# Performance work log

Measured on AMD Instinct MI355X. Metric: run time of the kernel, lower is better.

## Reference

```python
import jax, jax.numpy as jnp
import numpy as np

NUM_GRAPHS = 128

def _gcn_conv(x, W, b, src, dst, deg_inv_sqrt, n_nodes):
    # PyG GCNConv: h = X W; out[dst] += d^-1/2[src] * d^-1/2[dst] * h[src]; out += b
    h = x @ W
    norm = deg_inv_sqrt[src] * deg_inv_sqrt[dst]  # [E]
    msg = h[src] * norm[:, None]                  # [E, C]
    out = jax.ops.segment_sum(msg, dst, num_segments=n_nodes)
    return out + b


def setup_inputs() -> dict:
    key = jax.random.key(0)
    k1, k2, k3, k4, k5 = jax.random.split(key, 5)
    n_nodes, n_edges, c_in, c_hid = 50000, 800000, 256, 256
    x = jax.random.normal(k1, (n_nodes, c_in), dtype=jnp.float32)
    edge_index = jax.random.randint(k2, (2, n_edges), 0, n_nodes, dtype=jnp.int64)
    batch = jnp.sort(jax.random.randint(k3, (n_nodes,), 0, NUM_GRAPHS, dtype=jnp.int64))
    s1 = 1.0 / np.sqrt(c_in)
    s2 = 1.0 / np.sqrt(c_hid)
    W1 = jax.random.uniform(k4, (c_in, c_hid), jnp.float32, -s1, s1)
    b1 = jnp.zeros((c_hid,), jnp.float32)
    W2 = jax.random.uniform(k5, (c_hid, c_hid), jnp.float32, -s2, s2)
    b2 = jnp.zeros((c_hid,), jnp.float32)
    return {"x": x, "edge_index": edge_index, "batch": batch,
            "W1": W1, "b1": b1, "W2": W2, "b2": b2}


def reference(x, edge_index, batch, W1, b1, W2, b2):
    n_nodes = x.shape[0]
    # add self-loops (GCNConv default add_self_loops=True)
    loops = jnp.arange(n_nodes, dtype=edge_index.dtype)
    src = jnp.concatenate([edge_index[0], loops])
    dst = jnp.concatenate([edge_index[1], loops])
    deg = jax.ops.segment_sum(jnp.ones_like(dst, dtype=x.dtype), dst, num_segments=n_nodes)
    deg_inv_sqrt = jnp.where(deg > 0, jax.lax.rsqrt(deg), 0.0)

    h = jax.nn.relu(_gcn_conv(x, W1, b1, src, dst, deg_inv_sqrt, n_nodes))
    # dropout p=0.2 is identity in eval mode
    h = jax.nn.relu(_gcn_conv(h, W2, b2, src, dst, deg_inv_sqrt, n_nodes))

    # global mean pool over graph ids
    sums = jax.ops.segment_sum(h, batch, num_segments=NUM_GRAPHS)
    cnts = jax.ops.segment_sum(jnp.ones((n_nodes,), h.dtype), batch, num_segments=NUM_GRAPHS)
    return sums / jnp.maximum(cnts, 1.0)[:, None]
```

## Files before the change

### kernel.cpp

```cpp
#include <hip/hip_runtime.h>

#define NCH 256
#define NS  16

typedef short short8 __attribute__((ext_vector_type(8)));
typedef float f32x4  __attribute__((ext_vector_type(4)));

__device__ __forceinline__ float b2f(unsigned short u) {
    union { unsigned int i; float f; } x; x.i = ((unsigned int)u) << 16; return x.f;
}
__device__ __forceinline__ unsigned short f2b(float f) {
    unsigned int u = __float_as_uint(f);
    unsigned int r = (u + 0x7FFFu + ((u >> 16) & 1u)) >> 16;
    return (unsigned short)r;
}

__global__ __launch_bounds__(256) void k_init_deg(int* __restrict__ deg, int n) {
    int i = blockIdx.x * 256 + threadIdx.x;
    if (i < n) deg[i] = 1;
}

__global__ __launch_bounds__(256) void k_hist(const int* __restrict__ dst, int E,
                                              int* __restrict__ deg) {
    int e = blockIdx.x * 256 + threadIdx.x;
    if (e < E) atomicAdd(&deg[dst[e]], 1);
}

__global__ __launch_bounds__(256) void k_scan_blk(const int* __restrict__ deg,
                                                  int* __restrict__ part,
                                                  int* __restrict__ bsum, int N) {
    __shared__ int sm[256];
    int t = threadIdx.x;
    int base = blockIdx.x * 1024 + t * 4;
    int v[4]; int s = 0;
#pragma unroll
    for (int j = 0; j < 4; ++j) {
        int i = base + j;
        int d = (i < N) ? (deg[i] - 1) : 0;
        v[j] = d; s += d;
    }
    sm[t] = s; __syncthreads();
#pragma unroll
    for (int off = 1; off < 256; off <<= 1) {
        int u = (t >= off) ? sm[t - off] : 0;
        __syncthreads();
        sm[t] += u;
        __syncthreads();
    }
    int excl = sm[t] - s;
#pragma unroll
    for (int j = 0; j < 4; ++j) {
        int i = base + j;
        if (i < N) part[i] = excl;
        excl += v[j];
    }
    if (t == 255) bsum[blockIdx.x] = sm[255];
}

__global__ void k_scan_top(int* __restrict__ bsum, int nb, int* __restrict__ rowptr_end) {
    int t = threadIdx.x;
    int orig = (t < nb) ? bsum[t] : 0;
    int v = orig;
#pragma unroll
    for (int off = 1; off < 64; off <<= 1) {
        int u = __shfl_up(v, off, 64);
        if (t >= off) v += u;
    }
    if (t < nb) bsum[t] = v - orig;
    if (t == 63) *rowptr_end = v;
}

__global__ __launch_bounds__(256) void k_finalize(const int* __restrict__ deg,
                                                  int* __restrict__ row_ptr,
                                                  const int* __restrict__ boff,
                                                  int* __restrict__ cursor,
                                                  float* __restrict__ dinv, int N) {
    int i = blockIdx.x * 256 + threadIdx.x;
    if (i < N) {
        int rp = row_ptr[i] + boff[i >> 10];
        row_ptr[i] = rp;
        cursor[i]  = rp;
        dinv[i] = rsqrtf((float)deg[i]);
    }
}

__global__ __launch_bounds__(256) void k_scatter(const int* __restrict__ src,
                                                 const int* __restrict__ dst, int E,
                                                 int* __restrict__ cursor,
                                                 int* __restrict__ col) {
    int e = blockIdx.x * 256 + threadIdx.x;
    if (e < E) {
        int d = dst[e];
        int pos = atomicAdd(&cursor[d], 1);
        col[pos] = src[e];
    }
}

__global__ __launch_bounds__(256) void k_wprep(const int* __restrict__ col,
                                               const float* __restrict__ dinv,
                                               int2* __restrict__ cw, int E) {
    int i = blockIdx.x * 256 + threadIdx.x;
    if (i < E) {
        int s = col[i];
        cw[i] = make_int2(s, __float_as_int(dinv[s]));
    }
}

__global__ __launch_bounds__(256) void k_cast8(const float* __restrict__ in,
                                               unsigned short* __restrict__ out, int n8) {
    int i = blockIdx.x * 256 + threadIdx.x;
    if (i < n8) {
        const float4* p = (const float4*)(in + (size_t)i * 8);
        float4 a = p[0], b = p[1];
        unsigned short us[8];
        us[0] = f2b(a.x); us[1] = f2b(a.y); us[2] = f2b(a.z); us[3] = f2b(a.w);
        us[4] = f2b(b.x); us[5] = f2b(b.y); us[6] = f2b(b.z); us[7] = f2b(b.w);
        *(int4*)(out + (size_t)i * 8) = *(const int4*)us;
    }
}

__global__ __launch_bounds__(256) void k_castT(const float* __restrict__ W1,
                                               const float* __restrict__ W2,
                                               unsigned short* __restrict__ Wt1,
                                               unsigned short* __restrict__ Wt2) {
    int k = blockIdx.x, n = threadIdx.x;
    const float* W = blockIdx.y ? W2 : W1;
    unsigned short* Wt = blockIdx.y ? Wt2 : Wt1;
    Wt[(size_t)n * 256 + k] = f2b(W[(size_t)k * 256 + n]);
}

__device__ __forceinline__ void a_load(const unsigned short* __restrict__ A,
                                       int tile, int M, int lr, int ku, short8* dst) {
    int row = tile * 16 + lr; if (row >= M) row = M - 1;
    const unsigned short* pa = A + (size_t)row * NCH + ku * 8;
#pragma unroll
    for (int ks = 0; ks < 8; ++ks) dst[ks] = *(const short8*)(pa + ks * 32);
}

__global__ __launch_bounds__(256, 2) void k_gemm_rs(const unsigned short* __restrict__ A,
                                                    const unsigned short* __restrict__ Bt,
                                                    unsigned short* __restrict__ C, int M) {
    const int tid  = threadIdx.x;
    const int wid  = tid >> 6;
    const int lane = tid & 63;
    const int lr   = lane & 15;
    const int ku   = lane >> 4;

    short8 bfr[4][8];
    {
        const unsigned short* pb = Bt + (size_t)(wid * 64 + lr) * NCH + ku * 8;
#pragma unroll
        for (int nf = 0; nf < 4; ++nf)
#pragma unroll
            for (int ks = 0; ks < 8; ++ks)
                bfr[nf][ks] = *(const short8*)(pb + nf * 16 * NCH + ks * 32);
    }

    const int tiles = (M + 15) >> 4;
    int t = blockIdx.x;

    short8 afA[8], afB[8];
    if (t < tiles) a_load(A, t, M, lr, ku, afA);

    for (; t < tiles; t += gridDim.x) {
        int tn = t + gridDim.x;
        if (tn < tiles) a_load(A, tn, M, lr, ku, afB);

        f32x4 acc[4];
#pragma unroll
        for (int nf = 0; nf < 4; ++nf) acc[nf] = (f32x4){0.f, 0.f, 0.f, 0.f};

#pragma unroll
        for (int ks = 0; ks < 8; ++ks)
#pragma unroll
            for (int nf = 0; nf < 4; ++nf)
                acc[nf] = __builtin_amdgcn_mfma_f32_16x16x32_bf16(afA[ks], bfr[nf][ks],
                                                                  acc[nf], 0, 0, 0);

        int rb = t * 16 + ku * 4;
#pragma unroll
        for (int nf = 0; nf < 4; ++nf) {
            int col = wid * 64 + nf * 16 + lr;
#pragma unroll
            for (int r = 0; r < 4; ++r) {
                int row = rb + r;
                if (row < M) C[(size_t)row * NCH + col] = f2b(acc[nf][r]);
            }
        }
#pragma unroll
        for (int ks = 0; ks < 8; ++ks) afA[ks] = afB[ks];
    }
}

__global__ __launch_bounds__(256) void k_agg_w(const unsigned short* __restrict__ h,
                                               const float* __restrict__ dinv,
                                               const int* __restrict__ row_ptr,
                                               const int2* __restrict__ cw,
                                               const float* __restrict__ bias,
                                               unsigned short* __restrict__ out, int M) {
    int v = blockIdx.x * 4 + (threadIdx.x >> 6);
    if (v >= M) return;
    const int lane = threadIdx.x & 63;
    const int half = lane >> 5;
    const int cb   = (lane & 31) << 3;

    float acc[8] = {};
    float dv = dinv[v];

    int beg = row_ptr[v], end = row_ptr[v + 1];
    int i0 = beg + half * 2;

    short8 rs = {};
    if (half == 0) rs = *(const short8*)&h[(size_t)v * NCH + cb];

    short8 r0 = {}, r1 = {};
    float  w0 = 0.f, w1 = 0.f;
    bool b0 = i0 < end, b1 = i0 + 1 < end;
    if (b0) {
        int2 e = cw[i0];
        r0 = *(const short8*)&h[(size_t)e.x * NCH + cb];
        w0 = __int_as_float(e.y);
    }
    if (b1) {
        int2 e = cw[i0 + 1];
        r1 = *(const short8*)&h[(size_t)e.x * NCH + cb];
        w1 = __int_as_float(e.y);
    }

    while (b0) {
        int in = i0 + 4;
        bool n0 = in < end, n1 = in + 1 < end;
        short8 s0 = {}, s1 = {};
        float  x0 = 0.f, x1 = 0.f;
        if (n0) {
            int2 e = cw[in];
            s0 = *(const short8*)&h[(size_t)e.x * NCH + cb];
            x0 = __int_as_float(e.y);
        }
        if (n1) {
            int2 e = cw[in + 1];
            s1 = *(const short8*)&h[(size_t)e.x * NCH + cb];
            x1 = __int_as_float(e.y);
        }
#pragma unroll
        for (int i = 0; i < 8; ++i) acc[i] += w0 * b2f((unsigned short)r0[i]);
#pragma unroll
        for (int i = 0; i < 8; ++i) acc[i] += w1 * b2f((unsigned short)r1[i]);
        r0 = s0; r1 = s1; w0 = x0; w1 = x1; b0 = n0; b1 = n1; i0 = in;
    }

    if (half == 0) {
#pragma unroll
        for (int i = 0; i < 8; ++i) acc[i] += dv * b2f((unsigned short)rs[i]);
    }

#pragma unroll
    for (int i = 0; i < 8; ++i) acc[i] += __shfl_xor(acc[i], 32, 64);

    if (half == 0) {
        f32x4 bl = *(const f32x4*)&bias[cb];
        f32x4 bh = *(const f32x4*)&bias[cb + 4];
        unsigned short us[8];
#pragma unroll
        for (int i = 0; i < 8; ++i) {
            float b = (i < 4) ? bl[i] : bh[i - 4];
            us[i] = f2b(fmaxf(dv * acc[i] + b, 0.0f));
        }
        *(int4*)&out[(size_t)v * NCH + cb] = *(const int4*)us;
    }
}

__device__ __forceinline__ int lower_bound_i(const int* a, int n, int key) {
    int lo = 0, hi = n;
    while (lo < hi) {
        int mid = (lo + hi) >> 1;
        if (a[mid] < key) lo = mid + 1; else hi = mid;
    }
    return lo;
}

__global__ __launch_bounds__(64) void k_pool_a(const unsigned short* __restrict__ a,
                                               const int* __restrict__ batch,
                                               float* __restrict__ partial, int N) {
    int g = blockIdx.x, s = blockIdx.y;
    const int lane = threadIdx.x;
    const int half = lane >> 5;
    const int cb   = (lane & 31) << 3;

    int lo = lower_bound_i(batch, N, g);
    int hi = lower_bound_i(batch, N, g + 1);
    int cnt = hi - lo;
    int len = (cnt + NS - 1) / NS;
    int rlo = lo + s * len;
    int rhi = min(rlo + len, hi);

    float acc[8] = {};
    for (int r = rlo + half; r < rhi; r += 2) {
        short8 hv = *(const short8*)&a[(size_t)r * NCH + cb];
#pragma unroll
        for (int i = 0; i < 8; ++i) acc[i] += b2f((unsigned short)hv[i]);
    }
#pragma unroll
    for (int i = 0; i < 8; ++i) acc[i] += __shfl_xor(acc[i], 32, 64);

    if (half == 0) {
        float* p = partial + ((size_t)g * NS + s) * NCH + cb;
        *(f32x4*)p       = (f32x4){acc[0], acc[1], acc[2], acc[3]};
        *(f32x4*)(p + 4) = (f32x4){acc[4], acc[5], acc[6], acc[7]};
    }
}

__global__ __launch_bounds__(256) void k_pool_b(const float* __restrict__ partial,
                                                const int* __restrict__ batch,
                                                float* __restrict__ out, int N) {
    int g = blockIdx.x, ch = threadIdx.x;
    int lo = lower_bound_i(batch, N, g);
    int hi = lower_bound_i(batch, N, g + 1);
    float s = 0.0f;
#pragma unroll
    for (int k = 0; k < NS; ++k)
        s += partial[((size_t)g * NS + k) * NCH + ch];
    out[(size_t)g * NCH + ch] = s / (float)max(hi - lo, 1);
}

extern "C" void kernel_launch(void* const* d_in, const int* in_sizes, int n_in,
                              void* d_out, int out_size, void* d_ws, size_t ws_size,
                              hipStream_t stream) {
    const float* x     = (const float*)d_in[0];
    const int*   ei    = (const int*)d_in[1];
    const int*   batch = (const int*)d_in[2];
    const float* W1    = (const float*)d_in[3];
    const float* b1    = (const float*)d_in[4];
    const float* W2    = (const float*)d_in[5];
    const float* b2    = (const float*)d_in[6];
    float* out = (float*)d_out;

    const int M = in_sizes[0] / NCH;
    const int E = in_sizes[1] / 2;
    const int* src = ei;
    const int* dst = ei + E;

    char* w = (char*)d_ws;
    auto alloc = [&](size_t bytes) -> void* {
        void* p = (void*)w;
        w += (bytes + 255) & ~(size_t)255;
        return p;
    };
    int*   deg     = (int*)alloc((size_t)M * 4);
    float* dinv    = (float*)alloc((size_t)M * 4);
    int*   row_ptr = (int*)alloc((size_t)(M + 1) * 4);
    int*   cursor  = (int*)alloc((size_t)M * 4);
    int*   bsum    = (int*)alloc(64 * 4);
    int*   col     = (int*)alloc((size_t)E * 4);
    int2*  cw      = (int2*)alloc((size_t)E * 8);
    unsigned short* xb   = (unsigned short*)alloc((size_t)M * NCH * 2);
    unsigned short* bufP = (unsigned short*)alloc((size_t)M * NCH * 2);
    unsigned short* bufQ = (unsigned short*)alloc((size_t)M * NCH * 2);
    unsigned short* Wt1  = (unsigned short*)alloc((size_t)NCH * NCH * 2);
    unsigned short* Wt2  = (unsigned short*)alloc((size_t)NCH * NCH * 2);
    float* partial = (float*)alloc((size_t)128 * NS * NCH * 4);

    const int nb = (M + 1023) / 1024;

    k_cast8<<<(M * NCH / 8 + 255) / 256, 256, 0, stream>>>(x, xb, M * NCH / 8);
    k_castT<<<dim3(256, 2), 256, 0, stream>>>(W1, W2, Wt1, Wt2);

    k_init_deg<<<(M + 255) / 256, 256, 0, stream>>>(deg, M);
    k_hist<<<(E + 255) / 256, 256, 0, stream>>>(dst, E, deg);
    k_scan_blk<<<nb, 256, 0, stream>>>(deg, row_ptr, bsum, M);
    k_scan_top<<<1, 64, 0, stream>>>(bsum, nb, row_ptr + M);
    k_finalize<<<(M + 255) / 256, 256, 0, stream>>>(deg, row_ptr, bsum, cursor, dinv, M);
    k_scatter<<<(E + 255) / 256, 256, 0, stream>>>(src, dst, E, cursor, col);
    k_wprep<<<(E + 255) / 256, 256, 0, stream>>>(col, dinv, cw, E);

    const int ggrid = 512;

    k_gemm_rs<<<ggrid, 256, 0, stream>>>(xb, Wt1, bufP, M);
    k_agg_w<<<(M + 3) / 4, 256, 0, stream>>>(bufP, dinv, row_ptr, cw, b1, bufQ, M);
    k_gemm_rs<<<ggrid, 256, 0, stream>>>(bufQ, Wt2, bufP, M);
    k_agg_w<<<(M + 3) / 4, 256, 0, stream>>>(bufP, dinv, row_ptr, cw, b2, bufQ, M);
    k_pool_a<<<dim3(128, NS), 64, 0, stream>>>(bufQ, batch, partial, M);
    k_pool_b<<<128, 256, 0, stream>>>(partial, batch, out, M);
}
```

Before: 314.1 us.

## Fuse CSR weight prep into scatter, vectorize GEMM stores, deepen aggregation prefetch

Several changes land together. The separate weight-prep kernel is folded into the scatter kernel, and degree init is replaced by a memset, with the self-loop +1 applied in finalize. The GEMM swaps its MFMA operand order so each lane holds a row segment and can write 4 bf16 values per store instead of scalar stores, and its grid doubles to 1024. The aggregation loop now keeps 4 edges in flight per half-wave instead of 2, which raises memory-level parallelism at the cost of more registers.

```diff
diff --git a/kernel.cpp b/kernel.cpp
--- a/kernel.cpp
+++ b/kernel.cpp
@@ -13,11 +13,6 @@
     unsigned int u = __float_as_uint(f);
     unsigned int r = (u + 0x7FFFu + ((u >> 16) & 1u)) >> 16;
     return (unsigned short)r;
-}
-
-__global__ __launch_bounds__(256) void k_init_deg(int* __restrict__ deg, int n) {
-    int i = blockIdx.x * 256 + threadIdx.x;
-    if (i < n) deg[i] = 1;
 }
 
 __global__ __launch_bounds__(256) void k_hist(const int* __restrict__ dst, int E,
@@ -36,7 +31,7 @@
 #pragma unroll
     for (int j = 0; j < 4; ++j) {
         int i = base + j;
-        int d = (i < N) ? (deg[i] - 1) : 0;
+        int d = (i < N) ? deg[i] : 0;
         v[j] = d; s += d;
     }
     sm[t] = s; __syncthreads();
@@ -80,29 +75,21 @@
         int rp = row_ptr[i] + boff[i >> 10];
         row_ptr[i] = rp;
         cursor[i]  = rp;
-        dinv[i] = rsqrtf((float)deg[i]);
+        dinv[i] = rsqrtf((float)(deg[i] + 1));
     }
 }
 
 __global__ __launch_bounds__(256) void k_scatter(const int* __restrict__ src,
                                                  const int* __restrict__ dst, int E,
                                                  int* __restrict__ cursor,
-                                                 int* __restrict__ col) {
+                                                 const float* __restrict__ dinv,
+                                                 int2* __restrict__ cw) {
     int e = blockIdx.x * 256 + threadIdx.x;
     if (e < E) {
         int d = dst[e];
+        int s = src[e];
         int pos = atomicAdd(&cursor[d], 1);
-        col[pos] = src[e];
-    }
-}
-
-__global__ __launch_bounds__(256) void k_wprep(const int* __restrict__ col,
-                                               const float* __restrict__ dinv,
-                                               int2* __restrict__ cw, int E) {
-    int i = blockIdx.x * 256 + threadIdx.x;
-    if (i < E) {
-        int s = col[i];
-        cw[i] = make_int2(s, __float_as_int(dinv[s]));
+        cw[pos] = make_int2(s, __float_as_int(dinv[s]));
     }
 }
 
@@ -174,17 +161,18 @@
         for (int ks = 0; ks < 8; ++ks)
 #pragma unroll
             for (int nf = 0; nf < 4; ++nf)
-                acc[nf] = __builtin_amdgcn_mfma_f32_16x16x32_bf16(afA[ks], bfr[nf][ks],
+                acc[nf] = __builtin_amdgcn_mfma_f32_16x16x32_bf16(bfr[nf][ks], afA[ks],
                                                                   acc[nf], 0, 0, 0);
 
-        int rb = t * 16 + ku * 4;
-#pragma unroll
-        for (int nf = 0; nf < 4; ++nf) {
-            int col = wid * 64 + nf * 16 + lr;
-#pragma unroll
-            for (int r = 0; r < 4; ++r) {
-                int row = rb + r;
-                if (row < M) C[(size_t)row * NCH + col] = f2b(acc[nf][r]);
+        int row = t * 16 + lr;
+        if (row < M) {
+            unsigned short* pc = C + (size_t)row * NCH + wid * 64 + ku * 4;
+#pragma unroll
+            for (int nf = 0; nf < 4; ++nf) {
+                unsigned short us[4];
+                us[0] = f2b(acc[nf][0]); us[1] = f2b(acc[nf][1]);
+                us[2] = f2b(acc[nf][2]); us[3] = f2b(acc[nf][3]);
+                *(int2*)(pc + nf * 16) = *(const int2*)us;
             }
         }
 #pragma unroll
@@ -207,46 +195,46 @@
     float acc[8] = {};
     float dv = dinv[v];
 
-    int beg = row_ptr[v], end = row_ptr[v + 1];
-    int i0 = beg + half * 2;
-
     short8 rs = {};
     if (half == 0) rs = *(const short8*)&h[(size_t)v * NCH + cb];
 
-    short8 r0 = {}, r1 = {};
-    float  w0 = 0.f, w1 = 0.f;
-    bool b0 = i0 < end, b1 = i0 + 1 < end;
-    if (b0) {
-        int2 e = cw[i0];
-        r0 = *(const short8*)&h[(size_t)e.x * NCH + cb];
-        w0 = __int_as_float(e.y);
-    }
-    if (b1) {
-        int2 e = cw[i0 + 1];
-        r1 = *(const short8*)&h[(size_t)e.x * NCH + cb];
-        w1 = __int_as_float(e.y);
-    }
-
-    while (b0) {
-        int in = i0 + 4;
-        bool n0 = in < end, n1 = in + 1 < end;
-        short8 s0 = {}, s1 = {};
-        float  x0 = 0.f, x1 = 0.f;
-        if (n0) {
-            int2 e = cw[in];
-            s0 = *(const short8*)&h[(size_t)e.x * NCH + cb];
-            x0 = __int_as_float(e.y);
+    int beg = row_ptr[v], end = row_ptr[v + 1];
+    int i0 = beg + half * 4;
+
+    short8 r[4]; float wgt[4]; bool bv[4];
+#pragma unroll
+    for (int s = 0; s < 4; ++s) {
+        int idx = i0 + s;
+        bv[s] = idx < end;
+        r[s] = (short8){}; wgt[s] = 0.f;
+        if (bv[s]) {
+            int2 e = cw[idx];
+            r[s] = *(const short8*)&h[(size_t)e.x * NCH + cb];
+            wgt[s] = __int_as_float(e.y);
         }
-        if (n1) {
-            int2 e = cw[in + 1];
-            s1 = *(const short8*)&h[(size_t)e.x * NCH + cb];
-            x1 = __int_as_float(e.y);
+    }
+
+    while (bv[0]) {
+        int in = i0 + 8;
+        short8 rn[4]; float wn[4]; bool bn[4];
+#pragma unroll
+        for (int s = 0; s < 4; ++s) {
+            int idx = in + s;
+            bn[s] = idx < end;
+            rn[s] = (short8){}; wn[s] = 0.f;
+            if (bn[s]) {
+                int2 e = cw[idx];
+                rn[s] = *(const short8*)&h[(size_t)e.x * NCH + cb];
+                wn[s] = __int_as_float(e.y);
+            }
         }
 #pragma unroll
-        for (int i = 0; i < 8; ++i) acc[i] += w0 * b2f((unsigned short)r0[i]);
-#pragma unroll
-        for (int i = 0; i < 8; ++i) acc[i] += w1 * b2f((unsigned short)r1[i]);
-        r0 = s0; r1 = s1; w0 = x0; w1 = x1; b0 = n0; b1 = n1; i0 = in;
+        for (int s = 0; s < 4; ++s)
+#pragma unroll
+            for (int i = 0; i < 8; ++i) acc[i] += wgt[s] * b2f((unsigned short)r[s][i]);
+#pragma unroll
+        for (int s = 0; s < 4; ++s) { r[s] = rn[s]; wgt[s] = wn[s]; bv[s] = bn[s]; }
+        i0 = in;
     }
 
     if (half == 0) {
@@ -351,7 +339,6 @@
     int*   row_ptr = (int*)alloc((size_t)(M + 1) * 4);
     int*   cursor  = (int*)alloc((size_t)M * 4);
     int*   bsum    = (int*)alloc(64 * 4);
-    int*   col     = (int*)alloc((size_t)E * 4);
     int2*  cw      = (int2*)alloc((size_t)E * 8);
     unsigned short* xb   = (unsigned short*)alloc((size_t)M * NCH * 2);
     unsigned short* bufP = (unsigned short*)alloc((size_t)M * NCH * 2);
@@ -365,15 +352,14 @@
     k_cast8<<<(M * NCH / 8 + 255) / 256, 256, 0, stream>>>(x, xb, M * NCH / 8);
     k_castT<<<dim3(256, 2), 256, 0, stream>>>(W1, W2, Wt1, Wt2);
 
-    k_init_deg<<<(M + 255) / 256, 256, 0, stream>>>(deg, M);
+    hipMemsetAsync(deg, 0, (size_t)M * 4, stream);
     k_hist<<<(E + 255) / 256, 256, 0, stream>>>(dst, E, deg);
     k_scan_blk<<<nb, 256, 0, stream>>>(deg, row_ptr, bsum, M);
     k_scan_top<<<1, 64, 0, stream>>>(bsum, nb, row_ptr + M);
     k_finalize<<<(M + 255) / 256, 256, 0, stream>>>(deg, row_ptr, bsum, cursor, dinv, M);
-    k_scatter<<<(E + 255) / 256, 256, 0, stream>>>(src, dst, E, cursor, col);
-    k_wprep<<<(E + 255) / 256, 256, 0, stream>>>(col, dinv, cw, E);
-
-    const int ggrid = 512;
+    k_scatter<<<(E + 255) / 256, 256, 0, stream>>>(src, dst, E, cursor, dinv, cw);
+
+    const int ggrid = 1024;
 
     k_gemm_rs<<<ggrid, 256, 0, stream>>>(xb, Wt1, bufP, M);
     k_agg_w<<<(M + 3) / 4, 256, 0, stream>>>(bufP, dinv, row_ptr, cw, b1, bufQ, M);
```

Result: slower. 336.6 us (+7.2%).

## Fuse input cast into GEMM, merge scatter with weight prep, vectorize GEMM stores

Applied to the files above, without the earlier changes.

Removes the separate fp32-to-bf16 cast pass over x by converting inside the first GEMM's A-tile load. Merges the CSR scatter and the weight-prep pass so the packed (src, dinv) entries are written directly. Replaces the degree init kernel with a memset. Swaps the MFMA operand order so each lane writes 4 contiguous bf16 outputs as one 8-byte store instead of scattered 2-byte stores. Splits each aggregation launch into two half-range launches, which adds launch overhead with no clear benefit.

```diff
diff --git a/kernel.cpp b/kernel.cpp
--- a/kernel.cpp
+++ b/kernel.cpp
@@ -13,11 +13,6 @@
     unsigned int u = __float_as_uint(f);
     unsigned int r = (u + 0x7FFFu + ((u >> 16) & 1u)) >> 16;
     return (unsigned short)r;
-}
-
-__global__ __launch_bounds__(256) void k_init_deg(int* __restrict__ deg, int n) {
-    int i = blockIdx.x * 256 + threadIdx.x;
-    if (i < n) deg[i] = 1;
 }
 
 __global__ __launch_bounds__(256) void k_hist(const int* __restrict__ dst, int E,
@@ -36,7 +31,7 @@
 #pragma unroll
     for (int j = 0; j < 4; ++j) {
         int i = base + j;
-        int d = (i < N) ? (deg[i] - 1) : 0;
+        int d = (i < N) ? deg[i] : 0;
         v[j] = d; s += d;
     }
     sm[t] = s; __syncthreads();
@@ -80,42 +75,21 @@
         int rp = row_ptr[i] + boff[i >> 10];
         row_ptr[i] = rp;
         cursor[i]  = rp;
-        dinv[i] = rsqrtf((float)deg[i]);
+        dinv[i] = rsqrtf((float)(deg[i] + 1));
     }
 }
 
 __global__ __launch_bounds__(256) void k_scatter(const int* __restrict__ src,
                                                  const int* __restrict__ dst, int E,
                                                  int* __restrict__ cursor,
-                                                 int* __restrict__ col) {
+                                                 const float* __restrict__ dinv,
+                                                 int2* __restrict__ cw) {
     int e = blockIdx.x * 256 + threadIdx.x;
     if (e < E) {
         int d = dst[e];
+        int s = src[e];
         int pos = atomicAdd(&cursor[d], 1);
-        col[pos] = src[e];
-    }
-}
-
-__global__ __launch_bounds__(256) void k_wprep(const int* __restrict__ col,
-                                               const float* __restrict__ dinv,
-                                               int2* __restrict__ cw, int E) {
-    int i = blockIdx.x * 256 + threadIdx.x;
-    if (i < E) {
-        int s = col[i];
-        cw[i] = make_int2(s, __float_as_int(dinv[s]));
-    }
-}
-
-__global__ __launch_bounds__(256) void k_cast8(const float* __restrict__ in,
-                                               unsigned short* __restrict__ out, int n8) {
-    int i = blockIdx.x * 256 + threadIdx.x;
-    if (i < n8) {
-        const float4* p = (const float4*)(in + (size_t)i * 8);
-        float4 a = p[0], b = p[1];
-        unsigned short us[8];
-        us[0] = f2b(a.x); us[1] = f2b(a.y); us[2] = f2b(a.z); us[3] = f2b(a.w);
-        us[4] = f2b(b.x); us[5] = f2b(b.y); us[6] = f2b(b.z); us[7] = f2b(b.w);
-        *(int4*)(out + (size_t)i * 8) = *(const int4*)us;
+        cw[pos] = make_int2(s, __float_as_int(dinv[s]));
     }
 }
 
@@ -129,17 +103,35 @@
     Wt[(size_t)n * 256 + k] = f2b(W[(size_t)k * 256 + n]);
 }
 
-__device__ __forceinline__ void a_load(const unsigned short* __restrict__ A,
-                                       int tile, int M, int lr, int ku, short8* dst) {
+__device__ __forceinline__ void a_load_b(const unsigned short* __restrict__ A,
+                                         int tile, int M, int lr, int ku, short8* dst) {
     int row = tile * 16 + lr; if (row >= M) row = M - 1;
     const unsigned short* pa = A + (size_t)row * NCH + ku * 8;
 #pragma unroll
     for (int ks = 0; ks < 8; ++ks) dst[ks] = *(const short8*)(pa + ks * 32);
 }
 
-__global__ __launch_bounds__(256, 2) void k_gemm_rs(const unsigned short* __restrict__ A,
-                                                    const unsigned short* __restrict__ Bt,
-                                                    unsigned short* __restrict__ C, int M) {
+__device__ __forceinline__ void a_load_f(const float* __restrict__ A,
+                                         int tile, int M, int lr, int ku, short8* dst) {
+    int row = tile * 16 + lr; if (row >= M) row = M - 1;
+    const float* pa = A + (size_t)row * NCH + ku * 8;
+#pragma unroll
+    for (int ks = 0; ks < 8; ++ks) {
+        float4 f0 = *(const float4*)(pa + ks * 32);
+        float4 f1 = *(const float4*)(pa + ks * 32 + 4);
+        short8 v;
+        v[0] = (short)f2b(f0.x); v[1] = (short)f2b(f0.y);
+        v[2] = (short)f2b(f0.z); v[3] = (short)f2b(f0.w);
+        v[4] = (short)f2b(f1.x); v[5] = (short)f2b(f1.y);
+        v[6] = (short)f2b(f1.z); v[7] = (short)f2b(f1.w);
+        dst[ks] = v;
+    }
+}
+
+template <bool AF32>
+__device__ __forceinline__ void gemm_body(const void* __restrict__ Av,
+                                          const unsigned short* __restrict__ Bt,
+                                          unsigned short* __restrict__ C, int M) {
     const int tid  = threadIdx.x;
     const int wid  = tid >> 6;
     const int lane = tid & 63;
@@ -160,11 +152,17 @@
     int t = blockIdx.x;
 
     short8 afA[8], afB[8];
-    if (t < tiles) a_load(A, t, M, lr, ku, afA);
+    if (t < tiles) {
+        if (AF32) a_load_f((const float*)Av, t, M, lr, ku, afA);
+        else      a_load_b((const unsigned short*)Av, t, M, lr, ku, afA);
+    }
 
     for (; t < tiles; t += gridDim.x) {
         int tn = t + gridDim.x;
-        if (tn < tiles) a_load(A, tn, M, lr, ku, afB);
+        if (tn < tiles) {
+            if (AF32) a_load_f((const float*)Av, tn, M, lr, ku, afB);
+            else      a_load_b((const unsigned short*)Av, tn, M, lr, ku, afB);
+        }
 
         f32x4 acc[4];
 #pragma unroll
@@ -174,22 +172,35 @@
         for (int ks = 0; ks < 8; ++ks)
 #pragma unroll
             for (int nf = 0; nf < 4; ++nf)
-                acc[nf] = __builtin_amdgcn_mfma_f32_16x16x32_bf16(afA[ks], bfr[nf][ks],
+                acc[nf] = __builtin_amdgcn_mfma_f32_16x16x32_bf16(bfr[nf][ks], afA[ks],
                                                                   acc[nf], 0, 0, 0);
 
-        int rb = t * 16 + ku * 4;
-#pragma unroll
-        for (int nf = 0; nf < 4; ++nf) {
-            int col = wid * 64 + nf * 16 + lr;
-#pragma unroll
-            for (int r = 0; r < 4; ++r) {
-                int row = rb + r;
-                if (row < M) C[(size_t)row * NCH + col] = f2b(acc[nf][r]);
+        int row = t * 16 + lr;
+        if (row < M) {
+            unsigned short* pc = C + (size_t)row * NCH + wid * 64 + ku * 4;
+#pragma unroll
+            for (int nf = 0; nf < 4; ++nf) {
+                unsigned short us[4];
+                us[0] = f2b(acc[nf][0]); us[1] = f2b(acc[nf][1]);
+                us[2] = f2b(acc[nf][2]); us[3] = f2b(acc[nf][3]);
+                *(int2*)(pc + nf * 16) = *(const int2*)us;
             }
         }
 #pragma unroll
         for (int ks = 0; ks < 8; ++ks) afA[ks] = afB[ks];
     }
+}
+
+__global__ __launch_bounds__(256, 2) void k_gemm_f32in(const float* __restrict__ A,
+                                                       const unsigned short* __restrict__ Bt,
+                                                       unsigned short* __restrict__ C, int M) {
+    gemm_body<true>(A, Bt, C, M);
+}
+
+__global__ __launch_bounds__(256, 2) void k_gemm_rs(const unsigned short* __restrict__ A,
+                                                    const unsigned short* __restrict__ Bt,
+                                                    unsigned short* __restrict__ C, int M) {
+    gemm_body<false>(A, Bt, C, M);
 }
 
 __global__ __launch_bounds__(256) void k_agg_w(const unsigned short* __restrict__ h,
@@ -197,9 +208,10 @@
                                                const int* __restrict__ row_ptr,
                                                const int2* __restrict__ cw,
                                                const float* __restrict__ bias,
-                                               unsigned short* __restrict__ out, int M) {
-    int v = blockIdx.x * 4 + (threadIdx.x >> 6);
-    if (v >= M) return;
+                                               unsigned short* __restrict__ out,
+                                               int v0, int vend) {
+    int v = v0 + blockIdx.x * 4 + (threadIdx.x >> 6);
+    if (v >= vend) return;
     const int lane = threadIdx.x & 63;
     const int half = lane >> 5;
     const int cb   = (lane & 31) << 3;
@@ -207,11 +219,11 @@
     float acc[8] = {};
     float dv = dinv[v];
 
+    short8 rs = {};
+    if (half == 0) rs = *(const short8*)&h[(size_t)v * NCH + cb];
+
     int beg = row_ptr[v], end = row_ptr[v + 1];
     int i0 = beg + half * 2;
-
-    short8 rs = {};
-    if (half == 0) rs = *(const short8*)&h[(size_t)v * NCH + cb];
 
     short8 r0 = {}, r1 = {};
     float  w0 = 0.f, w1 = 0.f;
@@ -351,9 +363,7 @@
     int*   row_ptr = (int*)alloc((size_t)(M + 1) * 4);
     int*   cursor  = (int*)alloc((size_t)M * 4);
     int*   bsum    = (int*)alloc(64 * 4);
-    int*   col     = (int*)alloc((size_t)E * 4);
     int2*  cw      = (int2*)alloc((size_t)E * 8);
-    unsigned short* xb   = (unsigned short*)alloc((size_t)M * NCH * 2);
     unsigned short* bufP = (unsigned short*)alloc((size_t)M * NCH * 2);
     unsigned short* bufQ = (unsigned short*)alloc((size_t)M * NCH * 2);
     unsigned short* Wt1  = (unsigned short*)alloc((size_t)NCH * NCH * 2);
@@ -362,23 +372,25 @@
 
     const int nb = (M + 1023) / 1024;
 
-    k_cast8<<<(M * NCH / 8 + 255) / 256, 256, 0, stream>>>(x, xb, M * NCH / 8);
     k_castT<<<dim3(256, 2), 256, 0, stream>>>(W1, W2, Wt1, Wt2);
 
-    k_init_deg<<<(M + 255) / 256, 256, 0, stream>>>(deg, M);
+    hipMemsetAsync(deg, 0, (size_t)M * 4, stream);
     k_hist<<<(E + 255) / 256, 256, 0, stream>>>(dst, E, deg);
     k_scan_blk<<<nb, 256, 0, stream>>>(deg, row_ptr, bsum, M);
     k_scan_top<<<1, 64, 0, stream>>>(bsum, nb, row_ptr + M);
     k_finalize<<<(M + 255) / 256, 256, 0, stream>>>(deg, row_ptr, bsum, cursor, dinv, M);
-    k_scatter<<<(E + 255) / 256, 256, 0, stream>>>(src, dst, E, cursor, col);
-    k_wprep<<<(E + 255) / 256, 256, 0, stream>>>(col, dinv, cw, E);
+    k_scatter<<<(E + 255) / 256, 256, 0, stream>>>(src, dst, E, cursor, dinv, cw);
 
     const int ggrid = 512;
-
-    k_gemm_rs<<<ggrid, 256, 0, stream>>>(xb, Wt1, bufP, M);
-    k_agg_w<<<(M + 3) / 4, 256, 0, stream>>>(bufP, dinv, row_ptr, cw, b1, bufQ, M);
+    const int Mh = M / 2;
+    const int agrid = (Mh + 3) / 4;
+
+    k_gemm_f32in<<<ggrid, 256, 0, stream>>>(x, Wt1, bufP, M);
+    k_agg_w<<<agrid, 256, 0, stream>>>(bufP, dinv, row_ptr, cw, b1, bufQ, 0, Mh);
+    k_agg_w<<<(M - Mh + 3) / 4, 256, 0, stream>>>(bufP, dinv, row_ptr, cw, b1, bufQ, Mh, M);
     k_gemm_rs<<<ggrid, 256, 0, stream>>>(bufQ, Wt2, bufP, M);
-    k_agg_w<<<(M + 3) / 4, 256, 0, stream>>>(bufP, dinv, row_ptr, cw, b2, bufQ, M);
+    k_agg_w<<<agrid, 256, 0, stream>>>(bufP, dinv, row_ptr, cw, b2, bufQ, 0, Mh);
+    k_agg_w<<<(M - Mh + 3) / 4, 256, 0, stream>>>(bufP, dinv, row_ptr, cw, b2, bufQ, Mh, M);
     k_pool_a<<<dim3(128, NS), 64, 0, stream>>>(bufQ, batch, partial, M);
     k_pool_b<<<128, 256, 0, stream>>>(partial, batch, out, M);
 }
```

After: 320.0 us. About the same (+1.9%).

## Rewrite GEMM with LDS-staged A tiles, fuse scatter with weight prep, memset degrees

Applied to the files above, without the earlier changes.

The register-streamed GEMM is replaced by a 512-thread kernel. It stages 32-row A tiles into LDS through global_load_lds with an XOR swizzle and writes packed 4-element outputs. The CSR scatter and the weight-prep kernel are merged into one destination-sharded scatter that writes (src, dinv) pairs directly, which drops the intermediate col array. The sharding is meant to localise atomics. The degree init kernel becomes a memset, with the self-loop +1 moved into finalize. The sharded scatter reads the edge list eight times, and the new GEMM adds barriers per tile.

```diff
diff --git a/kernel.cpp b/kernel.cpp
--- a/kernel.cpp
+++ b/kernel.cpp
@@ -15,10 +15,9 @@
     return (unsigned short)r;
 }
 
-__global__ __launch_bounds__(256) void k_init_deg(int* __restrict__ deg, int n) {
-    int i = blockIdx.x * 256 + threadIdx.x;
-    if (i < n) deg[i] = 1;
-}
+#define GLOAD_LDS16(gptr, lptr) \
+    __builtin_amdgcn_global_load_lds((const __attribute__((address_space(1))) void*)(gptr), \
+                                     (__attribute__((address_space(3))) void*)(lptr), 16, 0, 0)
 
 __global__ __launch_bounds__(256) void k_hist(const int* __restrict__ dst, int E,
                                               int* __restrict__ deg) {
@@ -36,7 +35,7 @@
 #pragma unroll
     for (int j = 0; j < 4; ++j) {
         int i = base + j;
-        int d = (i < N) ? (deg[i] - 1) : 0;
+        int d = (i < N) ? deg[i] : 0;
         v[j] = d; s += d;
     }
     sm[t] = s; __syncthreads();
@@ -80,29 +79,30 @@
         int rp = row_ptr[i] + boff[i >> 10];
         row_ptr[i] = rp;
         cursor[i]  = rp;
-        dinv[i] = rsqrtf((float)deg[i]);
-    }
-}
-
-__global__ __launch_bounds__(256) void k_scatter(const int* __restrict__ src,
-                                                 const int* __restrict__ dst, int E,
-                                                 int* __restrict__ cursor,
-                                                 int* __restrict__ col) {
-    int e = blockIdx.x * 256 + threadIdx.x;
-    if (e < E) {
+        dinv[i] = rsqrtf((float)(deg[i] + 1));
+    }
+}
+
+__global__ __launch_bounds__(256) void k_scatter_sh(const int* __restrict__ src,
+                                                    const int* __restrict__ dst, int E,
+                                                    int* __restrict__ cursor,
+                                                    const float* __restrict__ dinv,
+                                                    int2* __restrict__ cw,
+                                                    unsigned shmul) {
+    const int shard  = blockIdx.x & 7;
+    const int nchunk = gridDim.x >> 3;
+    const int chunk  = blockIdx.x >> 3;
+    const int per = (E + nchunk - 1) / nchunk;
+    const int e0 = chunk * per;
+    const int e1 = min(e0 + per, E);
+    for (int e = e0 + threadIdx.x; e < e1; e += 256) {
         int d = dst[e];
-        int pos = atomicAdd(&cursor[d], 1);
-        col[pos] = src[e];
-    }
-}
-
-__global__ __launch_bounds__(256) void k_wprep(const int* __restrict__ col,
-                                               const float* __restrict__ dinv,
-                                               int2* __restrict__ cw, int E) {
-    int i = blockIdx.x * 256 + threadIdx.x;
-    if (i < E) {
-        int s = col[i];
-        cw[i] = make_int2(s, __float_as_int(dinv[s]));
+        int s = (int)__umulhi((unsigned)d, shmul);
+        if (s == shard) {
+            int sv = src[e];
+            int pos = atomicAdd(&cursor[d], 1);
+            cw[pos] = make_int2(sv, __float_as_int(dinv[sv]));
+        }
     }
 }
 
@@ -129,66 +129,76 @@
     Wt[(size_t)n * 256 + k] = f2b(W[(size_t)k * 256 + n]);
 }
 
-__device__ __forceinline__ void a_load(const unsigned short* __restrict__ A,
-                                       int tile, int M, int lr, int ku, short8* dst) {
-    int row = tile * 16 + lr; if (row >= M) row = M - 1;
-    const unsigned short* pa = A + (size_t)row * NCH + ku * 8;
-#pragma unroll
-    for (int ks = 0; ks < 8; ++ks) dst[ks] = *(const short8*)(pa + ks * 32);
-}
-
-__global__ __launch_bounds__(256, 2) void k_gemm_rs(const unsigned short* __restrict__ A,
-                                                    const unsigned short* __restrict__ Bt,
-                                                    unsigned short* __restrict__ C, int M) {
+__global__ __launch_bounds__(512, 4) void k_gemm_lds(const unsigned short* __restrict__ A,
+                                                     const unsigned short* __restrict__ Bt,
+                                                     unsigned short* __restrict__ C,
+                                                     int M, int tiles) {
+    __shared__ unsigned short As[32 * 256];
+
     const int tid  = threadIdx.x;
-    const int wid  = tid >> 6;
+    const int w    = tid >> 6;
     const int lane = tid & 63;
     const int lr   = lane & 15;
     const int ku   = lane >> 4;
 
-    short8 bfr[4][8];
+    short8 bfr[2][8];
     {
-        const unsigned short* pb = Bt + (size_t)(wid * 64 + lr) * NCH + ku * 8;
-#pragma unroll
-        for (int nf = 0; nf < 4; ++nf)
+        const unsigned short* pb = Bt + (size_t)(w * 32 + lr) * NCH + ku * 8;
+#pragma unroll
+        for (int nf = 0; nf < 2; ++nf)
 #pragma unroll
             for (int ks = 0; ks < 8; ++ks)
                 bfr[nf][ks] = *(const short8*)(pb + nf * 16 * NCH + ks * 32);
     }
 
-    const int tiles = (M + 15) >> 4;
-    int t = blockIdx.x;
-
-    short8 afA[8], afB[8];
-    if (t < tiles) a_load(A, t, M, lr, ku, afA);
-
-    for (; t < tiles; t += gridDim.x) {
-        int tn = t + gridDim.x;
-        if (tn < tiles) a_load(A, tn, M, lr, ku, afB);
-
-        f32x4 acc[4];
-#pragma unroll
-        for (int nf = 0; nf < 4; ++nf) acc[nf] = (f32x4){0.f, 0.f, 0.f, 0.f};
-
-#pragma unroll
-        for (int ks = 0; ks < 8; ++ks)
-#pragma unroll
-            for (int nf = 0; nf < 4; ++nf)
-                acc[nf] = __builtin_amdgcn_mfma_f32_16x16x32_bf16(afA[ks], bfr[nf][ks],
-                                                                  acc[nf], 0, 0, 0);
-
-        int rb = t * 16 + ku * 4;
-#pragma unroll
-        for (int nf = 0; nf < 4; ++nf) {
-            int col = wid * 64 + nf * 16 + lr;
-#pragma unroll
-            for (int r = 0; r < 4; ++r) {
-                int row = rb + r;
-                if (row < M) C[(size_t)row * NCH + col] = f2b(acc[nf][r]);
+    const int gu0 = w * 128 + lane;
+    for (int t = blockIdx.x; t < tiles; t += gridDim.x) {
+        __syncthreads();
+#pragma unroll
+        for (int j = 0; j < 2; ++j) {
+            int gu = gu0 + j * 64;
+            int r  = gu >> 5;
+            int u  = gu & 31;
+            int grow = t * 32 + r; if (grow >= M) grow = M - 1;
+            const unsigned short* gp = A + (size_t)grow * NCH + ((u ^ (r & 7)) << 3);
+            GLOAD_LDS16(gp, As + (size_t)(w * 128 + j * 64) * 8);
+        }
+        __syncthreads();
+
+        f32x4 acc[2][2];
+#pragma unroll
+        for (int rf = 0; rf < 2; ++rf)
+#pragma unroll
+            for (int nf = 0; nf < 2; ++nf) acc[rf][nf] = (f32x4){0.f, 0.f, 0.f, 0.f};
+
+#pragma unroll
+        for (int ks = 0; ks < 8; ++ks) {
+#pragma unroll
+            for (int rf = 0; rf < 2; ++rf) {
+                int row = rf * 16 + lr;
+                int uu  = (ks * 4 + ku) ^ (row & 7);
+                short8 af = *(const short8*)&As[row * 256 + uu * 8];
+                acc[rf][0] = __builtin_amdgcn_mfma_f32_16x16x32_bf16(bfr[0][ks], af,
+                                                                     acc[rf][0], 0, 0, 0);
+                acc[rf][1] = __builtin_amdgcn_mfma_f32_16x16x32_bf16(bfr[1][ks], af,
+                                                                     acc[rf][1], 0, 0, 0);
             }
         }
-#pragma unroll
-        for (int ks = 0; ks < 8; ++ks) afA[ks] = afB[ks];
+
+#pragma unroll
+        for (int rf = 0; rf < 2; ++rf) {
+            int row = t * 32 + rf * 16 + lr;
+            if (row < M) {
+                unsigned short* pc = C + (size_t)row * NCH + w * 32 + ku * 4;
+#pragma unroll
+                for (int nf = 0; nf < 2; ++nf) {
+                    unsigned short us[4];
+                    us[0] = f2b(acc[rf][nf][0]); us[1] = f2b(acc[rf][nf][1]);
+                    us[2] = f2b(acc[rf][nf][2]); us[3] = f2b(acc[rf][nf][3]);
+                    *(int2*)(pc + nf * 16) = *(const int2*)us;
+                }
+            }
+        }
     }
 }
 
@@ -207,11 +217,11 @@
     float acc[8] = {};
     float dv = dinv[v];
 
+    short8 rs = {};
+    if (half == 0) rs = *(const short8*)&h[(size_t)v * NCH + cb];
+
     int beg = row_ptr[v], end = row_ptr[v + 1];
     int i0 = beg + half * 2;
-
-    short8 rs = {};
-    if (half == 0) rs = *(const short8*)&h[(size_t)v * NCH + cb];
 
     short8 r0 = {}, r1 = {};
     float  w0 = 0.f, w1 = 0.f;
@@ -351,7 +361,6 @@
     int*   row_ptr = (int*)alloc((size_t)(M + 1) * 4);
     int*   cursor  = (int*)alloc((size_t)M * 4);
     int*   bsum    = (int*)alloc(64 * 4);
-    int*   col     = (int*)alloc((size_t)E * 4);
     int2*  cw      = (int2*)alloc((size_t)E * 8);
     unsigned short* xb   = (unsigned short*)alloc((size_t)M * NCH * 2);
     unsigned short* bufP = (unsigned short*)alloc((size_t)M * NCH * 2);
@@ -361,24 +370,26 @@
     float* partial = (float*)alloc((size_t)128 * NS * NCH * 4);
 
     const int nb = (M + 1023) / 1024;
+    const unsigned shmul = (unsigned)(((8ull << 32) + M - 1) / (unsigned long long)M);
+    const int tiles = (M + 31) / 32;
 
     k_cast8<<<(M * NCH / 8 + 255) / 256, 256, 0, stream>>>(x, xb, M * NCH / 8);
     k_castT<<<dim3(256, 2), 256, 0, stream>>>(W1, W2, Wt1, Wt2);
 
-    k_init_deg<<<(M + 255) / 256, 256, 0, stream>>>(deg, M);
+    hipMemsetAsync(deg, 0, (size_t)M * 4, stream);
     k_hist<<<(E + 255) / 256, 256, 0, stream>>>(dst, E, deg);
     k_scan_blk<<<nb, 256, 0, stream>>>(deg, row_ptr, bsum, M);
     k_scan_top<<<1, 64, 0, stream>>>(bsum, nb, row_ptr + M);
     k_finalize<<<(M + 255) / 256, 256, 0, stream>>>(deg, row_ptr, bsum, cursor, dinv, M);
-    k_scatter<<<(E + 255) / 256, 256, 0, stream>>>(src, dst, E, cursor, col);
-    k_wprep<<<(E + 255) / 256, 256, 0, stream>>>(col, dinv, cw, E);
+    k_scatter_sh<<<2048, 256, 0, stream>>>(src, dst, E, cursor, dinv, cw, shmul);
 
     const int ggrid = 512;
-
-    k_gemm_rs<<<ggrid, 256, 0, stream>>>(xb, Wt1, bufP, M);
-    k_agg_w<<<(M + 3) / 4, 256, 0, stream>>>(bufP, dinv, row_ptr, cw, b1, bufQ, M);
-    k_gemm_rs<<<ggrid, 256, 0, stream>>>(bufQ, Wt2, bufP, M);
-    k_agg_w<<<(M + 3) / 4, 256, 0, stream>>>(bufP, dinv, row_ptr, cw, b2, bufQ, M);
+    const int agrid = (M + 3) / 4;
+
+    k_gemm_lds<<<ggrid, 512, 0, stream>>>(xb, Wt1, bufP, M, tiles);
+    k_agg_w<<<agrid, 256, 0, stream>>>(bufP, dinv, row_ptr, cw, b1, bufQ, M);
+    k_gemm_lds<<<ggrid, 512, 0, stream>>>(bufQ, Wt2, bufP, M, tiles);
+    k_agg_w<<<agrid, 256, 0, stream>>>(bufP, dinv, row_ptr, cw, b2, bufQ, M);
     k_pool_a<<<dim3(128, NS), 64, 0, stream>>>(bufQ, batch, partial, M);
     k_pool_b<<<128, 256, 0, stream>>>(partial, batch, out, M);
 }
```

Result: faster. 287.7 us (-8.4%).
